# Kernel tuning notes

Hardware: AMD Instinct MI355X
Metric: run time of the kernel (lower is better)

## Reference

```python
import jax, jax.numpy as jnp
import numpy as np

K = 8          # num groups / object slots
FC = 256       # fc_size
LAST = 128     # last_fc_size
B = 2048       # batch
M = 1024       # input size
H = 512        # state (hidden) size


def _ln(x, g, b):
    # LayerNorm over last dim, eps matches torch default 1e-5
    mu = jnp.mean(x, axis=-1, keepdims=True)
    var = jnp.mean((x - mu) ** 2, axis=-1, keepdims=True)
    return (x - mu) * jax.lax.rsqrt(var + 1e-5) * g + b


def setup_inputs() -> dict:
    key = jax.random.key(0)
    ks = jax.random.split(key, 10)
    s = 0.05
    d = {
        "x": jax.random.normal(ks[0], (B * K, M), jnp.float32),
        "state": jax.random.normal(ks[1], (B * K, H), jnp.float32),
        # encoder: Linear(H->FC) + LN(FC)
        "enc_w": jax.random.normal(ks[2], (H, FC), jnp.float32) * s,
        "enc_b": jnp.zeros((FC,), jnp.float32),
        "enc_g": jnp.ones((FC,), jnp.float32),
        "enc_bb": jnp.zeros((FC,), jnp.float32),
        # core: Linear(2*FC->FC) + LN(FC)
        "core_w": jax.random.normal(ks[3], (2 * FC, FC), jnp.float32) * s,
        "core_b": jnp.zeros((FC,), jnp.float32),
        "core_g": jnp.ones((FC,), jnp.float32),
        "core_bb": jnp.zeros((FC,), jnp.float32),
        # context: Linear(FC->FC) + LN(FC)
        "ctx_w": jax.random.normal(ks[4], (FC, FC), jnp.float32) * s,
        "ctx_b": jnp.zeros((FC,), jnp.float32),
        "ctx_g": jnp.ones((FC,), jnp.float32),
        "ctx_bb": jnp.zeros((FC,), jnp.float32),
        # attention: Linear(FC->LAST) + LN(LAST) + Tanh + Linear(LAST->1) + Sigmoid
        "att1_w": jax.random.normal(ks[5], (FC, LAST), jnp.float32) * s,
        "att1_b": jnp.zeros((LAST,), jnp.float32),
        "att_g": jnp.ones((LAST,), jnp.float32),
        "att_bb": jnp.zeros((LAST,), jnp.float32),
        "att2_w": jax.random.normal(ks[6], (LAST, 1), jnp.float32) * s,
        "att2_b": jnp.zeros((1,), jnp.float32),
        # out_fc: Linear(FC + FC + M -> FC)
        "out_w": jax.random.normal(ks[7], (FC + FC + M, FC), jnp.float32) * s,
        "out_b": jnp.zeros((FC,), jnp.float32),
    }
    return d


def reference(x, state, enc_w, enc_b, enc_g, enc_bb,
              core_w, core_b, core_g, core_bb,
              ctx_w, ctx_b, ctx_g, ctx_bb,
              att1_w, att1_b, att_g, att_bb, att2_w, att2_b,
              out_w, out_b):
    bk, m = x.shape
    k = K
    b = bk // k
    # 0. encode state: [B*K, H] -> [B*K, FC]
    s1 = jax.nn.relu(_ln(state @ enc_w + enc_b, enc_g, enc_bb))
    h1 = s1.shape[-1]
    s1r = s1.reshape(b, k, h1)
    # focus: K-1 copies of each slot's state  [b, k, k-1, h1]
    fs = jnp.broadcast_to(s1r[:, :, None, :], (b, k, k - 1, h1))
    # context: gather the K-1 other slots' states (replaces torch python loop)
    idx = np.array([[j for j in range(k) if j != i] for i in range(k)])  # [k, k-1]
    cs = s1r[:, idx, :]  # [b, k, k-1, h1]
    concat = jnp.concatenate([fs, cs], axis=-1).reshape(b * k * (k - 1), 2 * h1)
    # core / context MLPs over pairs
    core = jax.nn.relu(_ln(concat @ core_w + core_b, core_g, core_bb))   # [b*k*(k-1), FC]
    ctx = jax.nn.relu(_ln(core @ ctx_w + ctx_b, ctx_g, ctx_bb))          # [b*k*(k-1), FC]
    # attention scalar per pair
    att_h = jnp.tanh(_ln(core @ att1_w + att1_b, att_g, att_bb))
    att = jax.nn.sigmoid(att_h @ att2_w + att2_b)                        # [b*k*(k-1), 1]
    # attention-weighted sum over the K-1 context dim
    h2 = ctx.shape[-1]
    effect = jnp.sum(ctx.reshape(b * k, k - 1, h2) * att.reshape(b * k, k - 1, 1), axis=1)
    # decode: concat encoded state, effect, input -> new state
    total = jnp.concatenate([s1, effect, x], axis=-1)
    new_state = total @ out_w + out_b
    return (new_state, new_state)
```

## Files before the change

### kernel.cpp

```cpp
#include <hip/hip_runtime.h>
#include <stdint.h>

#define FC    256
#define HH    512
#define MX    1024
#define LASTN 128
#define NROW  16384
#define NGRP  2048

typedef unsigned short u16;
typedef __bf16 bf16x8 __attribute__((ext_vector_type(8)));
typedef float  f32x4  __attribute__((ext_vector_type(4)));

__device__ __forceinline__ float red16(float v) {
#pragma unroll
  for (int m = 1; m < 16; m <<= 1) v += __shfl_xor(v, m);
  return v;
}
__device__ __forceinline__ u16 to_bf16(float f) {
  unsigned u = __float_as_uint(f);
  return (u16)((u + 0x8000u) >> 16);
}
__device__ __forceinline__ float from_bf16(u16 s) {
  return __uint_as_float(((unsigned)s) << 16);
}
__device__ __forceinline__ uint32_t pk2(float a, float b) {
  return (uint32_t)to_bf16(a) | ((uint32_t)to_bf16(b) << 16);
}
__device__ __forceinline__ float tanh_fast(float x) {
  float e = __expf(2.f * x);
  return __fdividef(e - 1.f, e + 1.f);
}
__device__ __forceinline__ float sigmoid_fast(float x) {
  return __fdividef(1.f, 1.f + __expf(-x));
}
__device__ __forceinline__ void glds16(const void* g, void* l) {
  __builtin_amdgcn_global_load_lds(
      (__attribute__((address_space(1))) uint32_t*)g,
      (__attribute__((address_space(3))) uint32_t*)l, 16, 0, 0);
}
__device__ __forceinline__ bf16x8 frag_ld(const u16* p) {
  return __builtin_bit_cast(bf16x8, *(const uint4*)p);
}

__global__ __launch_bounds__(256) void k_prep(
    const float* __restrict__ enc_w, const float* __restrict__ core_w,
    const float* __restrict__ ctx_w, const float* __restrict__ att1_w,
    const float* __restrict__ out_w,
    u16* __restrict__ encT, u16* __restrict__ uvT, u16* __restrict__ ctxT,
    u16* __restrict__ attT, u16* __restrict__ outT)
{
  const int bx = blockIdx.x, tid = threadIdx.x;
  const float* W; u16* D; int NKC, N, local; int uv = 0;
  if (bx < 64)       { W = enc_w;  D = encT; NKC = 16; N = 256; local = bx * 256 + tid; }
  else if (bx < 128) { W = core_w; D = uvT;  NKC = 8;  N = 256; local = (bx-64)*256 + tid; uv = 1; }
  else if (bx < 160) { W = ctx_w;  D = ctxT; NKC = 8;  N = 256; local = (bx-128)*256 + tid; }
  else if (bx < 176) { W = att1_w; D = attT; NKC = 8;  N = 128; local = (bx-160)*256 + tid; }
  else               { W = out_w;  D = outT; NKC = 48; N = 256; local = (bx-176)*256 + tid; }
  const int l  = local & 63;
  const int kc = (local >> 6) % NKC;
  const int u  = (local >> 6) / NKC;
  const int n  = u * 16 + (l & 15);
  const int k0 = kc * 32 + (l >> 4) * 8;
  float f[8];
#pragma unroll
  for (int j = 0; j < 8; ++j) {
    const int k = k0 + j;
    if (uv) f[j] = (n < 256) ? W[(size_t)k * 256 + n] : W[(size_t)(256 + k) * 256 + (n - 256)];
    else    f[j] = W[(size_t)k * N + n];
  }
  uint4 w;
  w.x = pk2(f[0], f[1]); w.y = pk2(f[2], f[3]);
  w.z = pk2(f[4], f[5]); w.w = pk2(f[6], f[7]);
  *(uint4*)&D[(size_t)local * 8] = w;
}

__global__ __launch_bounds__(256) void k_enc(
    const float* __restrict__ state, const u16* __restrict__ encT,
    const float* __restrict__ enc_b, const float* __restrict__ enc_g,
    const float* __restrict__ enc_bb, u16* __restrict__ s1b)
{
  __shared__ __align__(16) u16 smA[2][128 * 8];
  __shared__ __align__(16) u16 smB[2][16 * 64 * 8];
  __shared__ float smP[2][2][16][2];
  const int tid = threadIdx.x, wv = tid >> 6, lane = tid & 63;
  const int cl = lane & 15, quad = lane >> 4;
  const int rb = wv >> 1, cb = wv & 1;
  const int row0 = blockIdx.x * 32;
  f32x4 acc[8];
#pragma unroll
  for (int u = 0; u < 8; ++u) acc[u] = (f32x4){0.f, 0.f, 0.f, 0.f};

  for (int kk = 0; kk < 8; ++kk) {
    __syncthreads();
    {
      const int p = tid >> 7, lu = tid & 127;
      const int kc = kk * 2 + p;
      const int rblk = lu >> 6, ll = lu & 63;
      const float* src = state + (size_t)(row0 + rblk * 16 + (ll & 15)) * HH + kc * 32 + (ll >> 4) * 8;
      float4 a = *(const float4*)src, b = *(const float4*)(src + 4);
      uint4 w; w.x = pk2(a.x, a.y); w.y = pk2(a.z, a.w); w.z = pk2(b.x, b.y); w.w = pk2(b.z, b.w);
      *(uint4*)&smA[p][(size_t)lu * 8] = w;
    }
#pragma unroll
    for (int p = 0; p < 2; ++p)
#pragma unroll
      for (int i = 0; i < 4; ++i) {
        const int u = wv * 4 + i;
        glds16(encT + ((size_t)(u * 16 + kk * 2 + p) * 64 + lane) * 8, &smB[p][u * 512]);
      }
    __syncthreads();
#pragma unroll
    for (int p = 0; p < 2; ++p) {
      bf16x8 af = frag_ld(&smA[p][(rb * 64 + lane) * 8]);
#pragma unroll
      for (int u = 0; u < 8; ++u) {
        bf16x8 bf = frag_ld(&smB[p][((cb * 8 + u) * 64 + lane) * 8]);
        acc[u] = __builtin_amdgcn_mfma_f32_16x16x32_bf16(af, bf, acc[u], 0, 0, 0);
      }
    }
  }
  float bias[8], gg[8], bb[8];
#pragma unroll
  for (int u = 0; u < 8; ++u) {
    const int col = cb * 128 + u * 16 + cl;
    bias[u] = enc_b[col]; gg[u] = enc_g[col]; bb[u] = enc_bb[col];
  }
  float vv[4][8];
#pragma unroll
  for (int r4 = 0; r4 < 4; ++r4) {
    float s = 0.f, sq = 0.f;
#pragma unroll
    for (int u = 0; u < 8; ++u) {
      float v = acc[u][r4] + bias[u];
      vv[r4][u] = v; s += v; sq += v * v;
    }
    s = red16(s); sq = red16(sq);
    if (cl == 0) { smP[cb][rb][quad * 4 + r4][0] = s; smP[cb][rb][quad * 4 + r4][1] = sq; }
  }
  __syncthreads();
#pragma unroll
  for (int r4 = 0; r4 < 4; ++r4) {
    const int rr = quad * 4 + r4;
    const float S  = smP[0][rb][rr][0] + smP[1][rb][rr][0];
    const float SQ = smP[0][rb][rr][1] + smP[1][rb][rr][1];
    const float mu = S * (1.f / 256.f);
    const float rs = rsqrtf(SQ * (1.f / 256.f) - mu * mu + 1e-5f);
    const int row = row0 + rb * 16 + rr;
#pragma unroll
    for (int u = 0; u < 8; ++u) {
      float o = fmaxf((vv[r4][u] - mu) * rs * gg[u] + bb[u], 0.f);
      s1b[(size_t)row * FC + cb * 128 + u * 16 + cl] = to_bf16(o);
    }
  }
}

__global__ __launch_bounds__(256) void k_uv(
    const u16* __restrict__ s1b, const u16* __restrict__ uvT,
    float* __restrict__ UV)
{
  __shared__ __align__(16) u16 smA[2][4 * 64 * 8];
  __shared__ __align__(16) u16 smB[2][8 * 64 * 8];
  const int tid = threadIdx.x, wv = tid >> 6, lane = tid & 63;
  const int cl = lane & 15, quad = lane >> 4;
  const int row0 = blockIdx.x * 64;
  const int nb = blockIdx.y;
  f32x4 acc[8];
#pragma unroll
  for (int u = 0; u < 8; ++u) acc[u] = (f32x4){0.f, 0.f, 0.f, 0.f};

  for (int kk = 0; kk < 4; ++kk) {
    __syncthreads();
#pragma unroll
    for (int p = 0; p < 2; ++p) {
      const int kc = kk * 2 + p;
      glds16(s1b + (size_t)(row0 + wv * 16 + (lane & 15)) * FC + kc * 32 + (lane >> 4) * 8,
             &smA[p][wv * 512]);
#pragma unroll
      for (int i = 0; i < 2; ++i) {
        const int u = wv * 2 + i;
        glds16(uvT + ((size_t)((nb * 8 + u) * 8 + kc) * 64 + lane) * 8, &smB[p][u * 512]);
      }
    }
    __syncthreads();
#pragma unroll
    for (int p = 0; p < 2; ++p) {
      bf16x8 af = frag_ld(&smA[p][(wv * 64 + lane) * 8]);
#pragma unroll
      for (int u = 0; u < 8; ++u) {
        bf16x8 bf = frag_ld(&smB[p][(u * 64 + lane) * 8]);
        acc[u] = __builtin_amdgcn_mfma_f32_16x16x32_bf16(af, bf, acc[u], 0, 0, 0);
      }
    }
  }
#pragma unroll
  for (int r4 = 0; r4 < 4; ++r4) {
    const int row = row0 + wv * 16 + quad * 4 + r4;
#pragma unroll
    for (int u = 0; u < 8; ++u)
      UV[(size_t)row * 512 + nb * 128 + u * 16 + cl] = acc[u][r4];
  }
}

__global__ __launch_bounds__(256, 2) void k_pair(
    const float* __restrict__ UV, const float* __restrict__ core_b,
    const float* __restrict__ core_g, const float* __restrict__ core_bb,
    const u16* __restrict__ ctxT, const float* __restrict__ ctx_b,
    const float* __restrict__ ctx_g, const float* __restrict__ ctx_bb,
    const u16* __restrict__ attT, const float* __restrict__ att1_b,
    const float* __restrict__ att_g, const float* __restrict__ att_bb,
    const float* __restrict__ att2_w, const float* __restrict__ att2_b,
    u16* __restrict__ effb)
{
  __shared__ __align__(16) u16 smA[2048 * 8];
  __shared__ __align__(16) u16 smB[16 * 64 * 8];
  __shared__ __align__(16) float smUV[16 * 256];
  __shared__ float att_s[64];
  const int g = blockIdx.x;
  const int tid = threadIdx.x, wv = tid >> 6, lane = tid & 63;
  const int cl = lane & 15, quad = lane >> 4;

#pragma unroll
  for (int i = 0; i < 4; ++i) {
    const int r = wv * 4 + i;
    const int row = g * 8 + (r & 7);
    const int half = r >> 3;
    glds16(UV + (size_t)row * 512 + half * 256 + lane * 4, &smUV[r * 256]);
  }
#pragma unroll
  for (int i = 0; i < 8; ++i)
    *(uint4*)&smA[(size_t)(tid + i * 256) * 8] = (uint4){0u, 0u, 0u, 0u};
  __syncthreads();

  {
    const int sub = lane >> 4, cl16 = lane & 15;
    const int c0 = cl16 * 16;
    float4 CB[4], CG[4], CBB[4];
#pragma unroll
    for (int q = 0; q < 4; ++q) {
      CB[q]  = *(const float4*)&core_b[c0 + q * 4];
      CG[q]  = *(const float4*)&core_g[c0 + q * 4];
      CBB[q] = *(const float4*)&core_bb[c0 + q * 4];
    }
#pragma unroll
    for (int it = 0; it < 4; ++it) {
      const int p = it * 16 + wv * 4 + sub;
      if (p < 56) {
        const int i = p / 7, t = p - i * 7;
        const int j = t + (t >= i ? 1 : 0);
        const float* uA = &smUV[i * 256 + c0];
        const float* vB = &smUV[(8 + j) * 256 + c0];
        float v[16];
        float s = 0.f, sq = 0.f;
#pragma unroll
        for (int q = 0; q < 4; ++q) {
          float4 ua = *(const float4*)(uA + q * 4);
          float4 vb = *(const float4*)(vB + q * 4);
          float x0 = ua.x + vb.x + CB[q].x, x1 = ua.y + vb.y + CB[q].y;
          float x2 = ua.z + vb.z + CB[q].z, x3 = ua.w + vb.w + CB[q].w;
          v[q*4+0] = x0; v[q*4+1] = x1; v[q*4+2] = x2; v[q*4+3] = x3;
          s += x0 + x1 + x2 + x3;
          sq += x0*x0 + x1*x1 + x2*x2 + x3*x3;
        }
        s = red16(s); sq = red16(sq);
        const float mu = s * (1.f / 256.f);
        const float rs = rsqrtf(sq * (1.f / 256.f) - mu * mu + 1e-5f);
        float o[16];
#pragma unroll
        for (int q = 0; q < 4; ++q) {
          o[q*4+0] = fmaxf((v[q*4+0] - mu) * rs * CG[q].x + CBB[q].x, 0.f);
          o[q*4+1] = fmaxf((v[q*4+1] - mu) * rs * CG[q].y + CBB[q].y, 0.f);
          o[q*4+2] = fmaxf((v[q*4+2] - mu) * rs * CG[q].z + CBB[q].z, 0.f);
          o[q*4+3] = fmaxf((v[q*4+3] - mu) * rs * CG[q].w + CBB[q].w, 0.f);
        }
        const int base = ((p >> 4) * 8 + (cl16 >> 1)) * 64;
        const int lane1 = (p & 15) + 16 * ((cl16 & 1) * 2);
        uint4 w1, w2;
        w1.x = pk2(o[0], o[1]);  w1.y = pk2(o[2], o[3]);
        w1.z = pk2(o[4], o[5]);  w1.w = pk2(o[6], o[7]);
        w2.x = pk2(o[8], o[9]);  w2.y = pk2(o[10], o[11]);
        w2.z = pk2(o[12], o[13]); w2.w = pk2(o[14], o[15]);
        *(uint4*)&smA[(size_t)(base + lane1) * 8] = w1;
        *(uint4*)&smA[(size_t)(base + lane1 + 16) * 8] = w2;
      }
    }
  }
  __syncthreads();

  f32x4 accC[16], accT[8];
#pragma unroll
  for (int t = 0; t < 16; ++t) accC[t] = (f32x4){0.f, 0.f, 0.f, 0.f};
#pragma unroll
  for (int t = 0; t < 8; ++t)  accT[t] = (f32x4){0.f, 0.f, 0.f, 0.f};

  for (int kc = 0; kc < 8; ++kc) {
    if (kc) __syncthreads();
#pragma unroll
    for (int i = 0; i < 4; ++i) {
      const int q = wv * 4 + i;
      glds16(ctxT + ((size_t)(q * 8 + kc) * 64 + lane) * 8, &smB[q * 512]);
    }
    uint4 attf[8];
#pragma unroll
    for (int q = 0; q < 8; ++q)
      attf[q] = *(const uint4*)(attT + ((size_t)(q * 8 + kc) * 64 + lane) * 8);
    __syncthreads();
    bf16x8 af = frag_ld(&smA[((wv * 8 + kc) * 64 + lane) * 8]);
#pragma unroll
    for (int q = 0; q < 16; ++q) {
      bf16x8 bf = frag_ld(&smB[(q * 64 + lane) * 8]);
      accC[q] = __builtin_amdgcn_mfma_f32_16x16x32_bf16(af, bf, accC[q], 0, 0, 0);
    }
#pragma unroll
    for (int q = 0; q < 8; ++q) {
      bf16x8 bf = __builtin_bit_cast(bf16x8, attf[q]);
      accT[q] = __builtin_amdgcn_mfma_f32_16x16x32_bf16(af, bf, accT[q], 0, 0, 0);
    }
  }

  {
    float ab[8], ag[8], abb[8], aw[8];
#pragma unroll
    for (int t = 0; t < 8; ++t) {
      const int col = t * 16 + cl;
      ab[t] = att1_b[col]; ag[t] = att_g[col]; abb[t] = att_bb[col]; aw[t] = att2_w[col];
    }
    const float b2 = att2_b[0];
#pragma unroll
    for (int r4 = 0; r4 < 4; ++r4) {
      float v[8], s = 0.f, sq = 0.f;
#pragma unroll
      for (int t = 0; t < 8; ++t) {
        v[t] = accT[t][r4] + ab[t];
        s += v[t]; sq += v[t] * v[t];
      }
      s = red16(s); sq = red16(sq);
      const float mu = s * (1.f / 128.f);
      const float rs = rsqrtf(sq * (1.f / 128.f) - mu * mu + 1e-5f);
      float d = 0.f;
#pragma unroll
      for (int t = 0; t < 8; ++t) {
        float h = tanh_fast((v[t] - mu) * rs * ag[t] + abb[t]);
        d = fmaf(h, aw[t], d);
      }
      d = red16(d);
      if (cl == 0) {
        const int r = wv * 16 + quad * 4 + r4;
        if (r < 56) att_s[r] = sigmoid_fast(d + b2);
      }
    }
  }
  __syncthreads();

  u16* smS = smA;
  {
    float cb[16], cg[16], cbb[16];
#pragma unroll
    for (int t = 0; t < 16; ++t) {
      const int col = t * 16 + cl;
      cb[t] = ctx_b[col]; cg[t] = ctx_g[col]; cbb[t] = ctx_bb[col];
    }
#pragma unroll
    for (int r4 = 0; r4 < 4; ++r4) {
      float v[16], s = 0.f, sq = 0.f;
#pragma unroll
      for (int t = 0; t < 16; ++t) {
        v[t] = accC[t][r4] + cb[t];
        s += v[t]; sq += v[t] * v[t];
      }
      s = red16(s); sq = red16(sq);
      const float mu = s * (1.f / 256.f);
      const float rs = rsqrtf(sq * (1.f / 256.f) - mu * mu + 1e-5f);
      const int r = wv * 16 + quad * 4 + r4;
      if (r < 56) {
        const float ap = att_s[r];
#pragma unroll
        for (int t = 0; t < 16; ++t) {
          const int col = t * 16 + cl;
          float o = fmaxf((v[t] - mu) * rs * cg[t] + cbb[t], 0.f) * ap;
          smS[r * 264 + col] = to_bf16(o);
        }
      }
    }
  }
  __syncthreads();

  const int c = tid;
#pragma unroll
  for (int i = 0; i < 8; ++i) {
    float s = 0.f;
#pragma unroll
    for (int t2 = 0; t2 < 7; ++t2) s += from_bf16(smS[(i * 7 + t2) * 264 + c]);
    effb[(size_t)(g * 8 + i) * FC + c] = to_bf16(s);
  }
}

__global__ __launch_bounds__(256) void k_out(
    const u16* __restrict__ s1b, const u16* __restrict__ effb,
    const float* __restrict__ x, const u16* __restrict__ outT,
    const float* __restrict__ out_b, float* __restrict__ out, int dup)
{
  __shared__ __align__(16) u16 smA[2][4 * 64 * 8];
  __shared__ __align__(16) u16 smB[2][8 * 64 * 8];
  const int tid = threadIdx.x, wv = tid >> 6, lane = tid & 63;
  const int cl = lane & 15, quad = lane >> 4;
  const int row0 = blockIdx.x * 64;
  const int nb = blockIdx.y;
  f32x4 acc[8];
#pragma unroll
  for (int u = 0; u < 8; ++u) acc[u] = (f32x4){0.f, 0.f, 0.f, 0.f};

  for (int kk = 0; kk < 24; ++kk) {
    const int kc0 = kk * 2;
    __syncthreads();
    if (kc0 < 16) {
#pragma unroll
      for (int p = 0; p < 2; ++p) {
        const int kc = kc0 + p;
        const u16* base = (kc < 8) ? s1b : effb;
        const int kof = (kc & 7) * 32;
        glds16(base + (size_t)(row0 + wv * 16 + (lane & 15)) * FC + kof + (lane >> 4) * 8,
               &smA[p][wv * 512]);
      }
    } else {
      const int t = tid >> 6, ll = tid & 63;
      const float* src0 = x + (size_t)(row0 + t * 16 + (ll & 15)) * MX + (ll >> 4) * 8;
#pragma unroll
      for (int p = 0; p < 2; ++p) {
        const float* src = src0 + (kc0 + p - 16) * 32;
        float4 a = *(const float4*)src, b = *(const float4*)(src + 4);
        uint4 w; w.x = pk2(a.x, a.y); w.y = pk2(a.z, a.w); w.z = pk2(b.x, b.y); w.w = pk2(b.z, b.w);
        *(uint4*)&smA[p][(size_t)tid * 8] = w;
      }
    }
#pragma unroll
    for (int p = 0; p < 2; ++p)
#pragma unroll
      for (int i = 0; i < 2; ++i) {
        const int u = wv * 2 + i;
        glds16(outT + ((size_t)((nb * 8 + u) * 48 + kc0 + p) * 64 + lane) * 8, &smB[p][u * 512]);
      }
    __syncthreads();
#pragma unroll
    for (int p = 0; p < 2; ++p) {
      bf16x8 af = frag_ld(&smA[p][(wv * 64 + lane) * 8]);
#pragma unroll
      for (int u = 0; u < 8; ++u) {
        bf16x8 bf = frag_ld(&smB[p][(u * 64 + lane) * 8]);
        acc[u] = __builtin_amdgcn_mfma_f32_16x16x32_bf16(af, bf, acc[u], 0, 0, 0);
      }
    }
  }
  float bias[8];
#pragma unroll
  for (int u = 0; u < 8; ++u) bias[u] = out_b[nb * 128 + u * 16 + cl];
#pragma unroll
  for (int r4 = 0; r4 < 4; ++r4) {
    const int row = row0 + wv * 16 + quad * 4 + r4;
#pragma unroll
    for (int u = 0; u < 8; ++u) {
      const float o = acc[u][r4] + bias[u];
      const size_t off = (size_t)row * FC + nb * 128 + u * 16 + cl;
      out[off] = o;
      if (dup) out[(size_t)NROW * FC + off] = o;
    }
  }
}

extern "C" void kernel_launch(void* const* d_in, const int* in_sizes, int n_in,
                              void* d_out, int out_size, void* d_ws, size_t ws_size,
                              hipStream_t stream) {
  const float* x      = (const float*)d_in[0];
  const float* state  = (const float*)d_in[1];
  const float* enc_w  = (const float*)d_in[2];
  const float* enc_b  = (const float*)d_in[3];
  const float* enc_g  = (const float*)d_in[4];
  const float* enc_bb = (const float*)d_in[5];
  const float* core_w = (const float*)d_in[6];
  const float* core_b = (const float*)d_in[7];
  const float* core_g = (const float*)d_in[8];
  const float* core_bb= (const float*)d_in[9];
  const float* ctx_w  = (const float*)d_in[10];
  const float* ctx_b  = (const float*)d_in[11];
  const float* ctx_g  = (const float*)d_in[12];
  const float* ctx_bb = (const float*)d_in[13];
  const float* att1_w = (const float*)d_in[14];
  const float* att1_b = (const float*)d_in[15];
  const float* att_g  = (const float*)d_in[16];
  const float* att_bb = (const float*)d_in[17];
  const float* att2_w = (const float*)d_in[18];
  const float* att2_b = (const float*)d_in[19];
  const float* out_w  = (const float*)d_in[20];
  const float* out_b  = (const float*)d_in[21];

  char* ws = (char*)d_ws;
  float* UV  = (float*)ws;
  u16* s1b   = (u16*)(ws + 33554432);
  u16* effb  = (u16*)(ws + 41943040);
  u16* encT  = (u16*)(ws + 50331648);
  u16* uvT   = (u16*)(ws + 50593792);
  u16* ctxT  = (u16*)(ws + 50855936);
  u16* attT  = (u16*)(ws + 50987008);
  u16* outT  = (u16*)(ws + 51052544);
  float* out = (float*)d_out;
  const int dup = (out_size >= 2 * NROW * FC) ? 1 : 0;

  k_prep<<<dim3(368), 256, 0, stream>>>(enc_w, core_w, ctx_w, att1_w, out_w,
                                        encT, uvT, ctxT, attT, outT);
  k_enc<<<dim3(NROW / 32), 256, 0, stream>>>(state, encT, enc_b, enc_g, enc_bb, s1b);
  k_uv <<<dim3(NROW / 64, 4), 256, 0, stream>>>(s1b, uvT, UV);
  k_pair<<<dim3(NGRP), 256, 0, stream>>>(UV, core_b, core_g, core_bb,
                                         ctxT, ctx_b, ctx_g, ctx_bb,
                                         attT, att1_b, att_g, att_bb,
                                         att2_w, att2_b, effb);
  k_out<<<dim3(NROW / 64, 2), 256, 0, stream>>>(s1b, effb, x, outT, out_b, out, dup);
}
```

Measured before the change: 303.6 us.

## Alias LDS buffers, split att/ctx GEMM phases, swizzle smA for occupancy

Merges the UV staging buffer and the ctx weight tile into one shared allocation, cutting LDS per block so three blocks can fit per CU (launch bounds raised to 3). The attention GEMM and LayerNorm now finish before the ctx accumulators are allocated, which lowers peak register pressure. The core-LN pass is re-laned with XOR-rotated column chunks, and the bf16 A tile gets an XOR swizzle to reduce LDS bank conflicts. The risks are register spills under the tighter occupancy bound, and the extra serialization between the two GEMM phases.

```diff
diff --git a/kernel.cpp b/kernel.cpp
--- a/kernel.cpp
+++ b/kernel.cpp
@@ -15,6 +15,11 @@
 __device__ __forceinline__ float red16(float v) {
 #pragma unroll
   for (int m = 1; m < 16; m <<= 1) v += __shfl_xor(v, m);
+  return v;
+}
+__device__ __forceinline__ float red16hi(float v) {
+#pragma unroll
+  for (int m = 4; m < 64; m <<= 1) v += __shfl_xor(v, m);
   return v;
 }
 __device__ __forceinline__ u16 to_bf16(float f) {
@@ -202,7 +207,7 @@
   }
 }
 
-__global__ __launch_bounds__(256, 2) void k_pair(
+__global__ __launch_bounds__(256, 3) void k_pair(
     const float* __restrict__ UV, const float* __restrict__ core_b,
     const float* __restrict__ core_g, const float* __restrict__ core_bb,
     const u16* __restrict__ ctxT, const float* __restrict__ ctx_b,
@@ -213,12 +218,14 @@
     u16* __restrict__ effb)
 {
   __shared__ __align__(16) u16 smA[2048 * 8];
-  __shared__ __align__(16) u16 smB[16 * 64 * 8];
-  __shared__ __align__(16) float smUV[16 * 256];
+  __shared__ __align__(16) u16 smX[16 * 64 * 8];
   __shared__ float att_s[64];
+  float* smUV = (float*)smX;
+  u16*   smB  = smX;
   const int g = blockIdx.x;
   const int tid = threadIdx.x, wv = tid >> 6, lane = tid & 63;
   const int cl = lane & 15, quad = lane >> 4;
+  const int aswz = ((lane >> 5) & 1) << 2;
 
 #pragma unroll
   for (int i = 0; i < 4; ++i) {
@@ -233,18 +240,20 @@
   __syncthreads();
 
   {
-    const int sub = lane >> 4, cl16 = lane & 15;
-    const int c0 = cl16 * 16;
+    const int s4  = lane & 3;
+    const int g16 = lane >> 2;
+    const int c0  = g16 * 16;
     float4 CB[4], CG[4], CBB[4];
 #pragma unroll
     for (int q = 0; q < 4; ++q) {
-      CB[q]  = *(const float4*)&core_b[c0 + q * 4];
-      CG[q]  = *(const float4*)&core_g[c0 + q * 4];
-      CBB[q] = *(const float4*)&core_bb[c0 + q * 4];
+      const int cq = c0 + ((q ^ s4) << 2);
+      CB[q]  = *(const float4*)&core_b[cq];
+      CG[q]  = *(const float4*)&core_g[cq];
+      CBB[q] = *(const float4*)&core_bb[cq];
     }
 #pragma unroll
     for (int it = 0; it < 4; ++it) {
-      const int p = it * 16 + wv * 4 + sub;
+      const int p = it * 16 + wv * 4 + s4;
       if (p < 56) {
         const int i = p / 7, t = p - i * 7;
         const int j = t + (t >= i ? 1 : 0);
@@ -254,63 +263,51 @@
         float s = 0.f, sq = 0.f;
 #pragma unroll
         for (int q = 0; q < 4; ++q) {
-          float4 ua = *(const float4*)(uA + q * 4);
-          float4 vb = *(const float4*)(vB + q * 4);
+          const int qo = (q ^ s4) << 2;
+          float4 ua = *(const float4*)(uA + qo);
+          float4 vb = *(const float4*)(vB + qo);
           float x0 = ua.x + vb.x + CB[q].x, x1 = ua.y + vb.y + CB[q].y;
           float x2 = ua.z + vb.z + CB[q].z, x3 = ua.w + vb.w + CB[q].w;
           v[q*4+0] = x0; v[q*4+1] = x1; v[q*4+2] = x2; v[q*4+3] = x3;
           s += x0 + x1 + x2 + x3;
           sq += x0*x0 + x1*x1 + x2*x2 + x3*x3;
         }
-        s = red16(s); sq = red16(sq);
+        s = red16hi(s); sq = red16hi(sq);
         const float mu = s * (1.f / 256.f);
         const float rs = rsqrtf(sq * (1.f / 256.f) - mu * mu + 1e-5f);
-        float o[16];
 #pragma unroll
         for (int q = 0; q < 4; ++q) {
-          o[q*4+0] = fmaxf((v[q*4+0] - mu) * rs * CG[q].x + CBB[q].x, 0.f);
-          o[q*4+1] = fmaxf((v[q*4+1] - mu) * rs * CG[q].y + CBB[q].y, 0.f);
-          o[q*4+2] = fmaxf((v[q*4+2] - mu) * rs * CG[q].z + CBB[q].z, 0.f);
-          o[q*4+3] = fmaxf((v[q*4+3] - mu) * rs * CG[q].w + CBB[q].w, 0.f);
+          v[q*4+0] = fmaxf((v[q*4+0] - mu) * rs * CG[q].x + CBB[q].x, 0.f);
+          v[q*4+1] = fmaxf((v[q*4+1] - mu) * rs * CG[q].y + CBB[q].y, 0.f);
+          v[q*4+2] = fmaxf((v[q*4+2] - mu) * rs * CG[q].z + CBB[q].z, 0.f);
+          v[q*4+3] = fmaxf((v[q*4+3] - mu) * rs * CG[q].w + CBB[q].w, 0.f);
         }
-        const int base = ((p >> 4) * 8 + (cl16 >> 1)) * 64;
-        const int lane1 = (p & 15) + 16 * ((cl16 & 1) * 2);
-        uint4 w1, w2;
-        w1.x = pk2(o[0], o[1]);  w1.y = pk2(o[2], o[3]);
-        w1.z = pk2(o[4], o[5]);  w1.w = pk2(o[6], o[7]);
-        w2.x = pk2(o[8], o[9]);  w2.y = pk2(o[10], o[11]);
-        w2.z = pk2(o[12], o[13]); w2.w = pk2(o[14], o[15]);
-        *(uint4*)&smA[(size_t)(base + lane1) * 8] = w1;
-        *(uint4*)&smA[(size_t)(base + lane1 + 16) * 8] = w2;
+#pragma unroll
+        for (int q = 0; q < 4; ++q) {
+          const int lg = q ^ s4;
+          const int ks = (g16 * 2 + (lg >> 1)) & 3;
+          int slot = ((p >> 4) * 8 + (g16 >> 1)) * 64 + (p & 15) + 16 * ks;
+          slot ^= ((slot >> 5) & 1) << 2;
+          uint2 w;
+          w.x = pk2(v[q*4+0], v[q*4+1]);
+          w.y = pk2(v[q*4+2], v[q*4+3]);
+          *(uint2*)&smA[(size_t)slot * 8 + (lg & 1) * 4] = w;
+        }
       }
     }
   }
   __syncthreads();
 
-  f32x4 accC[16], accT[8];
-#pragma unroll
-  for (int t = 0; t < 16; ++t) accC[t] = (f32x4){0.f, 0.f, 0.f, 0.f};
-#pragma unroll
-  for (int t = 0; t < 8; ++t)  accT[t] = (f32x4){0.f, 0.f, 0.f, 0.f};
-
+  f32x4 accT[8];
+#pragma unroll
+  for (int t = 0; t < 8; ++t) accT[t] = (f32x4){0.f, 0.f, 0.f, 0.f};
+#pragma unroll 2
   for (int kc = 0; kc < 8; ++kc) {
-    if (kc) __syncthreads();
-#pragma unroll
-    for (int i = 0; i < 4; ++i) {
-      const int q = wv * 4 + i;
-      glds16(ctxT + ((size_t)(q * 8 + kc) * 64 + lane) * 8, &smB[q * 512]);
-    }
     uint4 attf[8];
 #pragma unroll
     for (int q = 0; q < 8; ++q)
       attf[q] = *(const uint4*)(attT + ((size_t)(q * 8 + kc) * 64 + lane) * 8);
-    __syncthreads();
-    bf16x8 af = frag_ld(&smA[((wv * 8 + kc) * 64 + lane) * 8]);
-#pragma unroll
-    for (int q = 0; q < 16; ++q) {
-      bf16x8 bf = frag_ld(&smB[(q * 64 + lane) * 8]);
-      accC[q] = __builtin_amdgcn_mfma_f32_16x16x32_bf16(af, bf, accC[q], 0, 0, 0);
-    }
+    bf16x8 af = frag_ld(&smA[(size_t)((((wv * 8 + kc) * 64) + lane) ^ aswz) * 8]);
 #pragma unroll
     for (int q = 0; q < 8; ++q) {
       bf16x8 bf = __builtin_bit_cast(bf16x8, attf[q]);
@@ -348,6 +345,25 @@
         const int r = wv * 16 + quad * 4 + r4;
         if (r < 56) att_s[r] = sigmoid_fast(d + b2);
       }
+    }
+  }
+
+  f32x4 accC[16];
+#pragma unroll
+  for (int t = 0; t < 16; ++t) accC[t] = (f32x4){0.f, 0.f, 0.f, 0.f};
+  for (int kc = 0; kc < 8; ++kc) {
+    if (kc) __syncthreads();
+#pragma unroll
+    for (int i = 0; i < 4; ++i) {
+      const int q = wv * 4 + i;
+      glds16(ctxT + ((size_t)(q * 8 + kc) * 64 + lane) * 8, &smB[q * 512]);
+    }
+    __syncthreads();
+    bf16x8 af = frag_ld(&smA[(size_t)((((wv * 8 + kc) * 64) + lane) ^ aswz) * 8]);
+#pragma unroll
+    for (int q = 0; q < 16; ++q) {
+      bf16x8 bf = frag_ld(&smB[(q * 64 + lane) * 8]);
+      accC[q] = __builtin_amdgcn_mfma_f32_16x16x32_bf16(af, bf, accC[q], 0, 0, 0);
     }
   }
   __syncthreads();
```

Result: faster. 290.3 us (-4.4%).
